# Kernel tuning notes

Hardware: AMD Instinct MI355X
Metric: run time of the kernel (lower is better)

## Reference

```python
import jax, jax.numpy as jnp
import numpy as np

B, S, D, H, HD = 2, 2048, 1024, 16, 64
SCALE = HD ** (-0.5)

def setup_inputs() -> dict:
    key = jax.random.key(0)
    ks = jax.random.split(key, 11)
    f = jax.random.normal
    return {
        "K_in": f(ks[0], (B, S, D), jnp.float32),
        "V_in": f(ks[1], (B, S, D), jnp.float32),
        "Q_in": f(ks[2], (B, S, D), jnp.float32),
        "Wk": f(ks[3], (H, D, HD), jnp.float32) * 0.02,
        "bk": f(ks[4], (H, HD), jnp.float32) * 0.02,
        "Wq": f(ks[5], (H, D, HD), jnp.float32) * 0.02,
        "bq": f(ks[6], (H, HD), jnp.float32) * 0.02,
        "Wv": f(ks[7], (H, D, HD), jnp.float32) * 0.02,
        "bv": f(ks[8], (H, HD), jnp.float32) * 0.02,
        "Wp": f(ks[9], (D, D), jnp.float32) * 0.02,
        "bp": f(ks[10], (D,), jnp.float32) * 0.02,
    }

def reference(K_in, V_in, Q_in, Wk, bk, Wq, bq, Wv, bv, Wp, bp):
    # Per-head linear projections (batched over heads): [B,H,S,HD]
    K = jnp.einsum('bsd,hde->bhse', K_in, Wk) + bk[None, :, None, :]
    Q = jnp.einsum('bsd,hde->bhse', Q_in, Wq) + bq[None, :, None, :]
    V = jnp.einsum('bsd,hde->bhse', V_in, Wv) + bv[None, :, None, :]
    # Attention scores [B,H,S,S], softmax over keys
    W = jax.nn.softmax(jnp.einsum('bhqe,bhke->bhqk', Q, K) * SCALE, axis=-1)
    val = jnp.einsum('bhqk,bhke->bhqe', W, V)            # [B,H,S,HD]
    # Concatenate heads along feature dim -> [B,S,H*HD] = [B,S,D]
    concat = jnp.transpose(val, (0, 2, 1, 3)).reshape(K_in.shape[0], K_in.shape[1], -1)
    return concat @ Wp.T + bp
```

## Files before the change

kernel.cpp:

```cpp
#include <hip/hip_runtime.h>
#include <hip/hip_bf16.h>
#include <math.h>

typedef float f32x4 __attribute__((ext_vector_type(4)));
typedef short s16x8 __attribute__((ext_vector_type(8)));
typedef unsigned short us16x4 __attribute__((ext_vector_type(4)));
typedef unsigned short us16x8 __attribute__((ext_vector_type(8)));
typedef unsigned int u32x2 __attribute__((ext_vector_type(2)));

#define MFMA16(a, b, c) __builtin_amdgcn_mfma_f32_16x16x32_bf16(a, b, c, 0, 0, 0)

static constexpr int B_ = 2, S_ = 2048, D_ = 1024, H_ = 16, HD_ = 64;
static constexpr float QSCALE = 0.125f * 1.44269504088896340736f;

__device__ __forceinline__ unsigned short f2bf(float f) {
    unsigned int u = __builtin_bit_cast(unsigned int, f);
    u += 0x7fffu + ((u >> 16) & 1);
    return (unsigned short)(u >> 16);
}

#if defined(__has_builtin) && __has_builtin(__builtin_amdgcn_cvt_pk_bf16_f32)
typedef __bf16 bf16x2v __attribute__((ext_vector_type(2)));
__device__ __forceinline__ unsigned int pk_bf16(float a, float b) {
    return __builtin_bit_cast(unsigned int, __builtin_amdgcn_cvt_pk_bf16_f32(a, b));
}
#else
__device__ __forceinline__ unsigned int pk_bf16(float a, float b) {
    return ((unsigned int)f2bf(a)) | (((unsigned int)f2bf(b)) << 16);
}
#endif

__device__ __forceinline__ void glds16(const unsigned short* g, unsigned short* l) {
    __builtin_amdgcn_global_load_lds(
        (const __attribute__((address_space(1))) void*)g,
        (__attribute__((address_space(3))) void*)l, 16, 0, 0);
}

__device__ __forceinline__ void glds16f(const float* g, float* l) {
    __builtin_amdgcn_global_load_lds(
        (const __attribute__((address_space(1))) void*)g,
        (__attribute__((address_space(3))) void*)l, 16, 0, 0);
}

__global__ __launch_bounds__(256) void transpose_w3(const float* __restrict__ W0,
                                                    const float* __restrict__ W1,
                                                    const float* __restrict__ W2,
                                                    unsigned short* __restrict__ Wt3) {
    const int z = blockIdx.z;
    const float* W = (z == 0) ? W0 : (z == 1) ? W1 : W2;
    unsigned short* dst = Wt3 + ((size_t)z << 20);
    const int h = blockIdx.x >> 2, dg = blockIdx.x & 3;
    const int lane = threadIdx.x & 63, w = threadIdx.x >> 6;
    const float* Wh = W + ((size_t)h << 16);
#pragma unroll
    for (int it = 0; it < 8; it++) {
        int d0 = dg * 256 + it * 32 + w * 8;
        us16x8 o;
#pragma unroll
        for (int j = 0; j < 8; j++) o[j] = f2bf(Wh[(d0 + j) * 64 + lane]);
        *(us16x8*)&dst[(size_t)(h * 64 + lane) * 1024 + d0] = o;
    }
}

__global__ __launch_bounds__(256) void gemm_qkv(const float* __restrict__ Qf,
                                                const float* __restrict__ Kf,
                                                const float* __restrict__ Vf,
                                                const unsigned short* __restrict__ Wt3,
                                                const float* __restrict__ bq,
                                                const float* __restrict__ bk,
                                                const float* __restrict__ bv,
                                                unsigned short* __restrict__ Qr,
                                                unsigned short* __restrict__ Kr,
                                                unsigned short* __restrict__ Vt) {
    __shared__ float Asf[128 * 64];
    __shared__ unsigned short Bs[128 * 64];
    const int flat = blockIdx.x + (blockIdx.y << 3) + (blockIdx.z << 8);
    const int wid = (flat & 7) * 96 + (flat >> 3);
    const int z = wid >> 8;
    const int by = (wid & 255) >> 3;
    const int bx = wid & 7;
    const float* A = (z == 0) ? Qf : (z == 1) ? Kf : Vf;
    const float* bias = (z == 0) ? bq : (z == 1) ? bk : bv;
    const int m0 = by * 128, n0 = bx * 128;

    const int tid = threadIdx.x;
    const int lane = tid & 63;
    const int w = tid >> 6, wm = w & 1, wn = w >> 1;
    const int l16 = lane & 15, quad = lane >> 4;
    const int arow = tid >> 4;
    const int su = (tid & 15) ^ arow;
    const float* Ag = A + (size_t)(m0 + arow) * 1024 + su * 4;
    float* Alf = Asf + tid * 4;
    const int srow = tid >> 3;
    const int sg = (tid & 7) ^ (srow & 7);
    const unsigned short* Bg = Wt3 + ((size_t)z << 20) + (size_t)(n0 + srow) * 1024 + sg * 8;
    unsigned short* Bl = Bs + tid * 8;
    const int xo8 = l16 & 7;

    f32x4 acc[4][4] = {};
    for (int k0 = 0; k0 < 1024; k0 += 64) {
        __syncthreads();
#pragma unroll
        for (int c = 0; c < 8; c++)
            glds16f(Ag + (size_t)c * 16 * 1024 + k0, Alf + c * 1024);
#pragma unroll
        for (int c = 0; c < 4; c++)
            glds16(Bg + (size_t)c * 32 * 1024 + k0, Bl + c * 2048);
        __syncthreads();
#pragma unroll
        for (int kc = 0; kc < 2; kc++) {
            s16x8 bf[4];
#pragma unroll
            for (int nt = 0; nt < 4; nt++)
                bf[nt] = *(const s16x8*)&Bs[(wn * 64 + nt * 16 + l16) * 64 +
                                            (((kc * 4 + quad) ^ xo8) * 8)];
#pragma unroll
            for (int mt = 0; mt < 4; mt++) {
                const int row = wm * 64 + mt * 16 + l16;
                const int u = kc * 8 + quad * 2;
                const int e = row & 15;
                f32x4 lo = *(const f32x4*)&Asf[row * 64 + ((u ^ e) * 4)];
                f32x4 hi = *(const f32x4*)&Asf[row * 64 + (((u + 1) ^ e) * 4)];
                s16x8 af;
                ((unsigned int*)&af)[0] = pk_bf16(lo[0], lo[1]);
                ((unsigned int*)&af)[1] = pk_bf16(lo[2], lo[3]);
                ((unsigned int*)&af)[2] = pk_bf16(hi[0], hi[1]);
                ((unsigned int*)&af)[3] = pk_bf16(hi[2], hi[3]);
#pragma unroll
                for (int nt = 0; nt < 4; nt++)
                    acc[mt][nt] = MFMA16(af, bf[nt], acc[mt][nt]);
            }
        }
    }

    const float scl = (z == 0) ? QSCALE : 1.0f;

    __syncthreads();
    unsigned short* T = ((unsigned short*)Asf) + w * 4096;
#pragma unroll
    for (int mt = 0; mt < 4; mt++)
#pragma unroll
        for (int nt = 0; nt < 4; nt++) {
            int nl = nt * 16 + l16;
            float bsv = bias[n0 + wn * 64 + nl];
#pragma unroll
            for (int r = 0; r < 4; r++) {
                int ml = mt * 16 + quad * 4 + r;
                unsigned short val = f2bf((acc[mt][nt][r] + bsv) * scl);
                int row = (z == 2) ? nl : ml;
                int col = (z == 2) ? ml : nl;
                T[row * 64 + (((col >> 3) ^ (row & 7)) * 8) + (col & 7)] = val;
            }
        }
#pragma unroll
    for (int it = 0; it < 8; it++) {
        int rr = it * 8 + (lane >> 3);
        int g = lane & 7;
        us16x8 vv = *(const us16x8*)&T[rr * 64 + ((g ^ (rr & 7)) * 8)];
        if (z == 2) {
            int n = n0 + wn * 64 + rr;
            int mb = m0 + wm * 64 + g * 8;
            int b = mb >> 11, s = mb & 2047;
            *(us16x8*)&Vt[(((size_t)(b * H_ + (n >> 6))) * HD_ + (n & 63)) * S_ + s] = vv;
        } else {
            unsigned short* dst = z ? Kr : Qr;
            *(us16x8*)&dst[(size_t)(m0 + wm * 64 + rr) * 1024 + n0 + wn * 64 + g * 8] = vv;
        }
    }
}

__global__ __launch_bounds__(256) void gemm_out(const unsigned short* __restrict__ A,
                                                const float* __restrict__ Wp,
                                                const float* __restrict__ bias,
                                                float* __restrict__ C) {
    __shared__ unsigned short As[128 * 64];
    __shared__ float Bsf[64 * 64];
    const int tid = threadIdx.x;
    const int lane = tid & 63;
    const int w = tid >> 6, wm = w & 1, wn = w >> 1;
    const int l16 = lane & 15, quad = lane >> 4;
    const int flat = blockIdx.x + (blockIdx.y << 4);
    const int wid = (flat & 7) * 64 + (flat >> 3);
    const int m0 = (wid >> 4) * 128, n0 = (wid & 15) * 64;
    const int srow = tid >> 3;
    const int sg = (tid & 7) ^ (srow & 7);
    const unsigned short* Ag = A + (size_t)(m0 + srow) * 1024 + sg * 8;
    unsigned short* Al = As + tid * 8;
    const int brow = tid >> 4;
    const int su = (tid & 15) ^ brow;
    const float* Bg = Wp + (size_t)(n0 + brow) * 1024 + su * 4;
    float* Blf = Bsf + tid * 4;
    const int xo8 = l16 & 7;

    f32x4 acc[4][2] = {};
    for (int k0 = 0; k0 < 1024; k0 += 64) {
        __syncthreads();
#pragma unroll
        for (int c = 0; c < 4; c++)
            glds16(Ag + (size_t)c * 32 * 1024 + k0, Al + c * 2048);
#pragma unroll
        for (int c = 0; c < 4; c++)
            glds16f(Bg + (size_t)c * 16 * 1024 + k0, Blf + c * 1024);
        __syncthreads();
#pragma unroll
        for (int kc = 0; kc < 2; kc++) {
            s16x8 bf[2];
#pragma unroll
            for (int nt = 0; nt < 2; nt++) {
                const int row = wn * 32 + nt * 16 + l16;
                const int u = kc * 8 + quad * 2;
                const int e = row & 15;
                f32x4 lo = *(const f32x4*)&Bsf[row * 64 + ((u ^ e) * 4)];
                f32x4 hi = *(const f32x4*)&Bsf[row * 64 + (((u + 1) ^ e) * 4)];
                ((unsigned int*)&bf[nt])[0] = pk_bf16(lo[0], lo[1]);
                ((unsigned int*)&bf[nt])[1] = pk_bf16(lo[2], lo[3]);
                ((unsigned int*)&bf[nt])[2] = pk_bf16(hi[0], hi[1]);
                ((unsigned int*)&bf[nt])[3] = pk_bf16(hi[2], hi[3]);
            }
#pragma unroll
            for (int mt = 0; mt < 4; mt++) {
                s16x8 af = *(const s16x8*)&As[(wm * 64 + mt * 16 + l16) * 64 +
                                              (((kc * 4 + quad) ^ xo8) * 8)];
#pragma unroll
                for (int nt = 0; nt < 2; nt++)
                    acc[mt][nt] = MFMA16(af, bf[nt], acc[mt][nt]);
            }
        }
    }
    const int lq = quad;
#pragma unroll
    for (int mt = 0; mt < 4; mt++)
#pragma unroll
        for (int nt = 0; nt < 2; nt++)
#pragma unroll
            for (int r = 0; r < 4; r++) {
                int mg = m0 + wm * 64 + mt * 16 + lq * 4 + r;
                int ng = n0 + wn * 32 + nt * 16 + l16;
                C[(size_t)mg * 1024 + ng] = acc[mt][nt][r] + bias[ng];
            }
}

__global__ __launch_bounds__(256) void flash_attn(const unsigned short* __restrict__ Qr,
                                                  const unsigned short* __restrict__ Kr,
                                                  const unsigned short* __restrict__ Vt,
                                                  unsigned short* __restrict__ Cc) {
    __shared__ unsigned short Ks[2][64 * 64];
    __shared__ unsigned short Vs[64 * 64];
    constexpr int LDT = 72;
    __shared__ unsigned short P4[4][16 * LDT];

    const int tid = threadIdx.x;
    const int lane = tid & 63, w = tid >> 6;
    const int l16 = lane & 15, quad = lane >> 4;
    const int bh = blockIdx.x, q0 = blockIdx.y * 64;
    const int b = bh >> 4, h = bh & 15;
    const int s_q = q0 + w * 16 + l16;

    const unsigned short* Qp = Qr + ((size_t)(b * S_ + s_q)) * D_ + h * HD_;

    const int srow = tid >> 3;
    const int sg = (tid & 7) ^ (srow & 7);
    const unsigned short* kg = Kr + ((size_t)(b * S_ + srow)) * D_ + h * HD_ + sg * 8;
    const unsigned short* vg = Vt + (((size_t)(b * H_ + h)) * HD_ + srow) * S_ + sg * 8;
    unsigned short* Vl = Vs + tid * 8;
    unsigned short* Pw = P4[w];
    const int pbase = l16 * LDT + quad * 4;
    const int xo = l16 & 7;

    glds16(kg, &Ks[0][tid * 8]);
    glds16(kg + (size_t)32 * D_, &Ks[0][tid * 8 + 2048]);
    kg += (size_t)64 * D_;

    s16x8 aq0 = *(const s16x8*)&Qp[quad * 8];
    s16x8 aq1 = *(const s16x8*)&Qp[32 + quad * 8];

    float l_part = 0.f;
    f32x4 o[4] = {};
    const f32x4 z4 = {0.f, 0.f, 0.f, 0.f};

    asm volatile("s_waitcnt vmcnt(0) lgkmcnt(0)\n\ts_barrier" ::: "memory");

    int cur = 0;
    for (int t = 0; t < 32; ++t) {
        const int last = (t == 31);
        glds16(vg, Vl);
        glds16(vg + (size_t)32 * S_, Vl + 2048);
        vg += 64;
        if (!last) {
            unsigned short* Kn = &Ks[cur ^ 1][tid * 8];
            glds16(kg, Kn);
            glds16(kg + (size_t)32 * D_, Kn + 2048);
            kg += (size_t)64 * D_;
        }

        const unsigned short* Kc_ = &Ks[cur][0];
        __builtin_amdgcn_s_setprio(1);
#pragma unroll
        for (int g = 0; g < 4; g++) {
            int row = g * 16 + l16;
            s16x8 kb0 = *(const s16x8*)&Kc_[row * 64 + ((quad ^ xo) * 8)];
            s16x8 kb1 = *(const s16x8*)&Kc_[row * 64 + (((4 + quad) ^ xo) * 8)];
            f32x4 sc = MFMA16(kb0, aq0, z4);
            sc = MFMA16(kb1, aq1, sc);
            float e0 = exp2f(sc[0]), e1 = exp2f(sc[1]);
            float e2 = exp2f(sc[2]), e3 = exp2f(sc[3]);
            l_part += (e0 + e1) + (e2 + e3);
            u32x2 pv;
            pv[0] = pk_bf16(e0, e1);
            pv[1] = pk_bf16(e2, e3);
            *(u32x2*)&Pw[pbase + g * 16] = pv;
        }
        __builtin_amdgcn_s_setprio(0);
        s16x8 pB0 = *(const s16x8*)&Pw[l16 * LDT + quad * 8];
        s16x8 pB1 = *(const s16x8*)&Pw[l16 * LDT + 32 + quad * 8];

        if (!last)
            asm volatile("s_waitcnt vmcnt(2)\n\ts_barrier" ::: "memory");
        else
            asm volatile("s_waitcnt vmcnt(0)\n\ts_barrier" ::: "memory");

        __builtin_amdgcn_s_setprio(1);
#pragma unroll
        for (int tt = 0; tt < 4; tt++) {
            int row = tt * 16 + l16;
            s16x8 v0 = *(const s16x8*)&Vs[row * 64 + ((quad ^ xo) * 8)];
            s16x8 v1 = *(const s16x8*)&Vs[row * 64 + (((4 + quad) ^ xo) * 8)];
            o[tt] = MFMA16(v0, pB0, o[tt]);
            o[tt] = MFMA16(v1, pB1, o[tt]);
        }
        __builtin_amdgcn_s_setprio(0);
        asm volatile("s_waitcnt vmcnt(0) lgkmcnt(0)\n\ts_barrier" ::: "memory");
        cur ^= 1;
    }

    float l = l_part;
    l += __shfl_xor(l, 16);
    l += __shfl_xor(l, 32);
    float rinv = 1.0f / l;
    unsigned short* Cp = Cc + ((size_t)(b * S_ + s_q)) * D_ + h * HD_;
#pragma unroll
    for (int t = 0; t < 4; t++) {
        u32x2 ov;
        ov[0] = pk_bf16(o[t][0] * rinv, o[t][1] * rinv);
        ov[1] = pk_bf16(o[t][2] * rinv, o[t][3] * rinv);
        *(u32x2*)&Cp[t * 16 + quad * 4] = ov;
    }
}

extern "C" void kernel_launch(void* const* d_in, const int* in_sizes, int n_in,
                              void* d_out, int out_size, void* d_ws, size_t ws_size,
                              hipStream_t stream) {
    const float* K_in = (const float*)d_in[0];
    const float* V_in = (const float*)d_in[1];
    const float* Q_in = (const float*)d_in[2];
    const float* Wk   = (const float*)d_in[3];
    const float* bk   = (const float*)d_in[4];
    const float* Wq   = (const float*)d_in[5];
    const float* bq   = (const float*)d_in[6];
    const float* Wv   = (const float*)d_in[7];
    const float* bv   = (const float*)d_in[8];
    const float* Wp   = (const float*)d_in[9];
    const float* bp   = (const float*)d_in[10];

    unsigned short* ws16 = (unsigned short*)d_ws;
    const size_t MC = 1u << 20;
    unsigned short* Wt3 = ws16;
    unsigned short* Qr  = Wt3 + 3 * MC;
    unsigned short* Kr  = Qr + 4 * MC;
    unsigned short* Vt  = Kr + 4 * MC;
    unsigned short* Cc  = Vt + 4 * MC;

    transpose_w3<<<dim3(64, 1, 3), 256, 0, stream>>>(Wq, Wk, Wv, Wt3);

    gemm_qkv<<<dim3(8, 32, 3), 256, 0, stream>>>(Q_in, K_in, V_in, Wt3, bq, bk, bv,
                                                 Qr, Kr, Vt);

    flash_attn<<<dim3(32, 32), 256, 0, stream>>>(Qr, Kr, Vt, Cc);

    gemm_out<<<dim3(16, 32), 256, 0, stream>>>(Cc, Wp, bp, (float*)d_out);
}
```

Baseline: 253.3 us.

## Shrink attention blocks to two waves and drop K double-buffering

The flash attention kernel now runs 128-thread blocks covering 32 queries each, launching twice as many blocks, and loads K and V with four 16-row chunks per thread. The K double buffer is removed, so shared memory per block is cut roughly in half and more blocks can share a CU. The cost is that K loads are no longer prefetched one tile ahead: each iteration loads K and V, waits on K, computes scores, then waits on V. Each block also re-streams the full K/V for a smaller query tile, which doubles global traffic for K and V.

```diff
diff --git a/kernel.cpp b/kernel.cpp
--- a/kernel.cpp
+++ b/kernel.cpp
@@ -240,66 +240,58 @@
             }
 }
 
-__global__ __launch_bounds__(256) void flash_attn(const unsigned short* __restrict__ Qr,
+__global__ __launch_bounds__(128) void flash_attn(const unsigned short* __restrict__ Qr,
                                                   const unsigned short* __restrict__ Kr,
                                                   const unsigned short* __restrict__ Vt,
                                                   unsigned short* __restrict__ Cc) {
-    __shared__ unsigned short Ks[2][64 * 64];
+    __shared__ unsigned short Ks[64 * 64];
     __shared__ unsigned short Vs[64 * 64];
     constexpr int LDT = 72;
-    __shared__ unsigned short P4[4][16 * LDT];
+    __shared__ unsigned short P2[2][16 * LDT];
 
     const int tid = threadIdx.x;
     const int lane = tid & 63, w = tid >> 6;
     const int l16 = lane & 15, quad = lane >> 4;
-    const int bh = blockIdx.x, q0 = blockIdx.y * 64;
+    const int bh = blockIdx.x, q0 = blockIdx.y * 32;
     const int b = bh >> 4, h = bh & 15;
     const int s_q = q0 + w * 16 + l16;
 
     const unsigned short* Qp = Qr + ((size_t)(b * S_ + s_q)) * D_ + h * HD_;
+    s16x8 aq0 = *(const s16x8*)&Qp[quad * 8];
+    s16x8 aq1 = *(const s16x8*)&Qp[32 + quad * 8];
 
     const int srow = tid >> 3;
     const int sg = (tid & 7) ^ (srow & 7);
     const unsigned short* kg = Kr + ((size_t)(b * S_ + srow)) * D_ + h * HD_ + sg * 8;
     const unsigned short* vg = Vt + (((size_t)(b * H_ + h)) * HD_ + srow) * S_ + sg * 8;
+    unsigned short* Kl = Ks + tid * 8;
     unsigned short* Vl = Vs + tid * 8;
-    unsigned short* Pw = P4[w];
+    unsigned short* Pw = P2[w];
     const int pbase = l16 * LDT + quad * 4;
     const int xo = l16 & 7;
-
-    glds16(kg, &Ks[0][tid * 8]);
-    glds16(kg + (size_t)32 * D_, &Ks[0][tid * 8 + 2048]);
-    kg += (size_t)64 * D_;
-
-    s16x8 aq0 = *(const s16x8*)&Qp[quad * 8];
-    s16x8 aq1 = *(const s16x8*)&Qp[32 + quad * 8];
 
     float l_part = 0.f;
     f32x4 o[4] = {};
     const f32x4 z4 = {0.f, 0.f, 0.f, 0.f};
 
-    asm volatile("s_waitcnt vmcnt(0) lgkmcnt(0)\n\ts_barrier" ::: "memory");
-
-    int cur = 0;
     for (int t = 0; t < 32; ++t) {
-        const int last = (t == 31);
-        glds16(vg, Vl);
-        glds16(vg + (size_t)32 * S_, Vl + 2048);
+        asm volatile("s_barrier" ::: "memory");
+#pragma unroll
+        for (int c = 0; c < 4; c++)
+            glds16(kg + (size_t)(c * 16) * D_, Kl + c * 1024);
+#pragma unroll
+        for (int c = 0; c < 4; c++)
+            glds16(vg + (size_t)(c * 16) * S_, Vl + c * 1024);
+        kg += (size_t)64 * D_;
         vg += 64;
-        if (!last) {
-            unsigned short* Kn = &Ks[cur ^ 1][tid * 8];
-            glds16(kg, Kn);
-            glds16(kg + (size_t)32 * D_, Kn + 2048);
-            kg += (size_t)64 * D_;
-        }
-
-        const unsigned short* Kc_ = &Ks[cur][0];
+        asm volatile("s_waitcnt vmcnt(4)\n\ts_barrier" ::: "memory");
+
         __builtin_amdgcn_s_setprio(1);
 #pragma unroll
         for (int g = 0; g < 4; g++) {
             int row = g * 16 + l16;
-            s16x8 kb0 = *(const s16x8*)&Kc_[row * 64 + ((quad ^ xo) * 8)];
-            s16x8 kb1 = *(const s16x8*)&Kc_[row * 64 + (((4 + quad) ^ xo) * 8)];
+            s16x8 kb0 = *(const s16x8*)&Ks[row * 64 + ((quad ^ xo) * 8)];
+            s16x8 kb1 = *(const s16x8*)&Ks[row * 64 + (((4 + quad) ^ xo) * 8)];
             f32x4 sc = MFMA16(kb0, aq0, z4);
             sc = MFMA16(kb1, aq1, sc);
             float e0 = exp2f(sc[0]), e1 = exp2f(sc[1]);
@@ -314,10 +306,7 @@
         s16x8 pB0 = *(const s16x8*)&Pw[l16 * LDT + quad * 8];
         s16x8 pB1 = *(const s16x8*)&Pw[l16 * LDT + 32 + quad * 8];
 
-        if (!last)
-            asm volatile("s_waitcnt vmcnt(2)\n\ts_barrier" ::: "memory");
-        else
-            asm volatile("s_waitcnt vmcnt(0)\n\ts_barrier" ::: "memory");
+        asm volatile("s_waitcnt vmcnt(0)\n\ts_barrier" ::: "memory");
 
         __builtin_amdgcn_s_setprio(1);
 #pragma unroll
@@ -329,8 +318,6 @@
             o[tt] = MFMA16(v1, pB1, o[tt]);
         }
         __builtin_amdgcn_s_setprio(0);
-        asm volatile("s_waitcnt vmcnt(0) lgkmcnt(0)\n\ts_barrier" ::: "memory");
-        cur ^= 1;
     }
 
     float l = l_part;
@@ -375,7 +362,7 @@
     gemm_qkv<<<dim3(8, 32, 3), 256, 0, stream>>>(Q_in, K_in, V_in, Wt3, bq, bk, bv,
                                                  Qr, Kr, Vt);
 
-    flash_attn<<<dim3(32, 32), 256, 0, stream>>>(Qr, Kr, Vt, Cc);
+    flash_attn<<<dim3(32, 64), 128, 0, stream>>>(Qr, Kr, Vt, Cc);
 
     gemm_out<<<dim3(16, 32), 256, 0, stream>>>(Cc, Wp, bp, (float*)d_out);
 }
```

Result: slower. 290.5 us (+14.7%).

## Double-buffer QKV and output GEMMs with register-staged fp32-to-bf16 conversion

Applied to the files above, without the earlier changes.

Both projection GEMMs now keep two LDS buffers and prefetch the next k-tile while the current one feeds the MFMAs, with one barrier per iteration instead of two. The fp32 operand is no longer copied into LDS as fp32 and converted by every reader. Each thread loads it into registers, converts it to bf16 once, and stores it into the next LDS buffer after the compute. This cuts LDS traffic and removes redundant conversions, at the cost of more registers and LDS, which could lower occupancy.

```diff
diff --git a/kernel.cpp b/kernel.cpp
--- a/kernel.cpp
+++ b/kernel.cpp
@@ -36,10 +36,13 @@
         (__attribute__((address_space(3))) void*)l, 16, 0, 0);
 }
 
-__device__ __forceinline__ void glds16f(const float* g, float* l) {
-    __builtin_amdgcn_global_load_lds(
-        (const __attribute__((address_space(1))) void*)g,
-        (__attribute__((address_space(3))) void*)l, 16, 0, 0);
+__device__ __forceinline__ us16x8 cvt8(const f32x4 lo, const f32x4 hi) {
+    us16x8 o;
+    ((unsigned int*)&o)[0] = pk_bf16(lo[0], lo[1]);
+    ((unsigned int*)&o)[1] = pk_bf16(lo[2], lo[3]);
+    ((unsigned int*)&o)[2] = pk_bf16(hi[0], hi[1]);
+    ((unsigned int*)&o)[3] = pk_bf16(hi[2], hi[3]);
+    return o;
 }
 
 __global__ __launch_bounds__(256) void transpose_w3(const float* __restrict__ W0,
@@ -72,8 +75,8 @@
                                                 unsigned short* __restrict__ Qr,
                                                 unsigned short* __restrict__ Kr,
                                                 unsigned short* __restrict__ Vt) {
-    __shared__ float Asf[128 * 64];
-    __shared__ unsigned short Bs[128 * 64];
+    __shared__ unsigned short As[2][128 * 64];
+    __shared__ unsigned short Bs[2][128 * 64];
     const int flat = blockIdx.x + (blockIdx.y << 3) + (blockIdx.z << 8);
     const int wid = (flat & 7) * 96 + (flat >> 3);
     const int z = wid >> 8;
@@ -87,56 +90,67 @@
     const int lane = tid & 63;
     const int w = tid >> 6, wm = w & 1, wn = w >> 1;
     const int l16 = lane & 15, quad = lane >> 4;
-    const int arow = tid >> 4;
-    const int su = (tid & 15) ^ arow;
-    const float* Ag = A + (size_t)(m0 + arow) * 1024 + su * 4;
-    float* Alf = Asf + tid * 4;
     const int srow = tid >> 3;
     const int sg = (tid & 7) ^ (srow & 7);
+    const float* Ag = A + (size_t)(m0 + srow) * 1024 + sg * 8;
     const unsigned short* Bg = Wt3 + ((size_t)z << 20) + (size_t)(n0 + srow) * 1024 + sg * 8;
-    unsigned short* Bl = Bs + tid * 8;
-    const int xo8 = l16 & 7;
-
+    const int xo = l16 & 7;
+
+    f32x4 ar[4][2];
     f32x4 acc[4][4] = {};
-    for (int k0 = 0; k0 < 1024; k0 += 64) {
-        __syncthreads();
-#pragma unroll
-        for (int c = 0; c < 8; c++)
-            glds16f(Ag + (size_t)c * 16 * 1024 + k0, Alf + c * 1024);
-#pragma unroll
-        for (int c = 0; c < 4; c++)
-            glds16(Bg + (size_t)c * 32 * 1024 + k0, Bl + c * 2048);
-        __syncthreads();
+
+#pragma unroll
+    for (int c = 0; c < 4; c++) {
+        ar[c][0] = *(const f32x4*)(Ag + (size_t)c * 32 * 1024);
+        ar[c][1] = *(const f32x4*)(Ag + (size_t)c * 32 * 1024 + 4);
+        glds16(Bg + (size_t)c * 32 * 1024, &Bs[0][tid * 8 + c * 2048]);
+    }
+#pragma unroll
+    for (int c = 0; c < 4; c++)
+        *(us16x8*)&As[0][tid * 8 + c * 2048] = cvt8(ar[c][0], ar[c][1]);
+    __syncthreads();
+
+    for (int t = 0; t < 16; ++t) {
+        const int cur = t & 1, nxt = cur ^ 1;
+        const int k0n = (t + 1) * 64;
+        if (t < 15) {
+#pragma unroll
+            for (int c = 0; c < 4; c++) {
+                ar[c][0] = *(const f32x4*)(Ag + (size_t)c * 32 * 1024 + k0n);
+                ar[c][1] = *(const f32x4*)(Ag + (size_t)c * 32 * 1024 + k0n + 4);
+            }
+#pragma unroll
+            for (int c = 0; c < 4; c++)
+                glds16(Bg + (size_t)c * 32 * 1024 + k0n, &Bs[nxt][tid * 8 + c * 2048]);
+        }
 #pragma unroll
         for (int kc = 0; kc < 2; kc++) {
             s16x8 bf[4];
 #pragma unroll
             for (int nt = 0; nt < 4; nt++)
-                bf[nt] = *(const s16x8*)&Bs[(wn * 64 + nt * 16 + l16) * 64 +
-                                            (((kc * 4 + quad) ^ xo8) * 8)];
+                bf[nt] = *(const s16x8*)&Bs[cur][(wn * 64 + nt * 16 + l16) * 64 +
+                                                 (((kc * 4 + quad) ^ xo) * 8)];
 #pragma unroll
             for (int mt = 0; mt < 4; mt++) {
-                const int row = wm * 64 + mt * 16 + l16;
-                const int u = kc * 8 + quad * 2;
-                const int e = row & 15;
-                f32x4 lo = *(const f32x4*)&Asf[row * 64 + ((u ^ e) * 4)];
-                f32x4 hi = *(const f32x4*)&Asf[row * 64 + (((u + 1) ^ e) * 4)];
-                s16x8 af;
-                ((unsigned int*)&af)[0] = pk_bf16(lo[0], lo[1]);
-                ((unsigned int*)&af)[1] = pk_bf16(lo[2], lo[3]);
-                ((unsigned int*)&af)[2] = pk_bf16(hi[0], hi[1]);
-                ((unsigned int*)&af)[3] = pk_bf16(hi[2], hi[3]);
+                s16x8 af = *(const s16x8*)&As[cur][(wm * 64 + mt * 16 + l16) * 64 +
+                                                   (((kc * 4 + quad) ^ xo) * 8)];
 #pragma unroll
                 for (int nt = 0; nt < 4; nt++)
                     acc[mt][nt] = MFMA16(af, bf[nt], acc[mt][nt]);
             }
         }
+        if (t < 15) {
+#pragma unroll
+            for (int c = 0; c < 4; c++)
+                *(us16x8*)&As[nxt][tid * 8 + c * 2048] = cvt8(ar[c][0], ar[c][1]);
+        }
+        __syncthreads();
     }
 
     const float scl = (z == 0) ? QSCALE : 1.0f;
 
     __syncthreads();
-    unsigned short* T = ((unsigned short*)Asf) + w * 4096;
+    unsigned short* T = ((unsigned short*)As) + w * 4096;
 #pragma unroll
     for (int mt = 0; mt < 4; mt++)
 #pragma unroll
@@ -173,8 +187,8 @@
                                                 const float* __restrict__ Wp,
                                                 const float* __restrict__ bias,
                                                 float* __restrict__ C) {
-    __shared__ unsigned short As[128 * 64];
-    __shared__ float Bsf[64 * 64];
+    __shared__ unsigned short As[2][128 * 64];
+    __shared__ unsigned short Bs[2][64 * 64];
     const int tid = threadIdx.x;
     const int lane = tid & 63;
     const int w = tid >> 6, wm = w & 1, wn = w >> 1;
@@ -185,47 +199,60 @@
     const int srow = tid >> 3;
     const int sg = (tid & 7) ^ (srow & 7);
     const unsigned short* Ag = A + (size_t)(m0 + srow) * 1024 + sg * 8;
-    unsigned short* Al = As + tid * 8;
-    const int brow = tid >> 4;
-    const int su = (tid & 15) ^ brow;
-    const float* Bg = Wp + (size_t)(n0 + brow) * 1024 + su * 4;
-    float* Blf = Bsf + tid * 4;
-    const int xo8 = l16 & 7;
-
+    const float* Bg = Wp + (size_t)(n0 + srow) * 1024 + sg * 8;
+    const int xo = l16 & 7;
+
+    f32x4 br[2][2];
     f32x4 acc[4][2] = {};
-    for (int k0 = 0; k0 < 1024; k0 += 64) {
-        __syncthreads();
-#pragma unroll
-        for (int c = 0; c < 4; c++)
-            glds16(Ag + (size_t)c * 32 * 1024 + k0, Al + c * 2048);
-#pragma unroll
-        for (int c = 0; c < 4; c++)
-            glds16f(Bg + (size_t)c * 16 * 1024 + k0, Blf + c * 1024);
-        __syncthreads();
+
+#pragma unroll
+    for (int c = 0; c < 2; c++) {
+        br[c][0] = *(const f32x4*)(Bg + (size_t)c * 32 * 1024);
+        br[c][1] = *(const f32x4*)(Bg + (size_t)c * 32 * 1024 + 4);
+    }
+#pragma unroll
+    for (int c = 0; c < 4; c++)
+        glds16(Ag + (size_t)c * 32 * 1024, &As[0][tid * 8 + c * 2048]);
+#pragma unroll
+    for (int c = 0; c < 2; c++)
+        *(us16x8*)&Bs[0][tid * 8 + c * 2048] = cvt8(br[c][0], br[c][1]);
+    __syncthreads();
+
+    for (int t = 0; t < 16; ++t) {
+        const int cur = t & 1, nxt = cur ^ 1;
+        const int k0n = (t + 1) * 64;
+        if (t < 15) {
+#pragma unroll
+            for (int c = 0; c < 2; c++) {
+                br[c][0] = *(const f32x4*)(Bg + (size_t)c * 32 * 1024 + k0n);
+                br[c][1] = *(const f32x4*)(Bg + (size_t)c * 32 * 1024 + k0n + 4);
+            }
+#pragma unroll
+            for (int c = 0; c < 4; c++)
+                glds16(Ag + (size_t)c * 32 * 1024 + k0n, &As[nxt][tid * 8 + c * 2048]);
+        }
 #pragma unroll
         for (int kc = 0; kc < 2; kc++) {
             s16x8 bf[2];
 #pragma unroll
-            for (int nt = 0; nt < 2; nt++) {
-                const int row = wn * 32 + nt * 16 + l16;
-                const int u = kc * 8 + quad * 2;
-                const int e = row & 15;
-                f32x4 lo = *(const f32x4*)&Bsf[row * 64 + ((u ^ e) * 4)];
-                f32x4 hi = *(const f32x4*)&Bsf[row * 64 + (((u + 1) ^ e) * 4)];
-                ((unsigned int*)&bf[nt])[0] = pk_bf16(lo[0], lo[1]);
-                ((unsigned int*)&bf[nt])[1] = pk_bf16(lo[2], lo[3]);
-                ((unsigned int*)&bf[nt])[2] = pk_bf16(hi[0], hi[1]);
-                ((unsigned int*)&bf[nt])[3] = pk_bf16(hi[2], hi[3]);
-            }
+            for (int nt = 0; nt < 2; nt++)
+                bf[nt] = *(const s16x8*)&Bs[cur][(wn * 32 + nt * 16 + l16) * 64 +
+                                                 (((kc * 4 + quad) ^ xo) * 8)];
 #pragma unroll
             for (int mt = 0; mt < 4; mt++) {
-                s16x8 af = *(const s16x8*)&As[(wm * 64 + mt * 16 + l16) * 64 +
-                                              (((kc * 4 + quad) ^ xo8) * 8)];
+                s16x8 af = *(const s16x8*)&As[cur][(wm * 64 + mt * 16 + l16) * 64 +
+                                                   (((kc * 4 + quad) ^ xo) * 8)];
 #pragma unroll
                 for (int nt = 0; nt < 2; nt++)
                     acc[mt][nt] = MFMA16(af, bf[nt], acc[mt][nt]);
             }
         }
+        if (t < 15) {
+#pragma unroll
+            for (int c = 0; c < 2; c++)
+                *(us16x8*)&Bs[nxt][tid * 8 + c * 2048] = cvt8(br[c][0], br[c][1]);
+        }
+        __syncthreads();
     }
     const int lq = quad;
 #pragma unroll
```

Result: slower. 282.0 us (+11.3%).
